# Performance work log

Hardware: AMD Instinct MI355X
Metric: run time of the kernel (lower is better)

Reference implementation:

```python
import jax, jax.numpy as jnp
import numpy as np

T1, T2 = 10.0, 50.0          # Canny hysteresis thresholds from EdgeNorm
HYST_ITERS = 16              # fixed-iteration approximation of Canny hysteresis BFS
TEMPERATURE = 1.0
NUM_CLASSES_M1 = 13.0


def _shift(a, dy, dx):
    # zero-padded shift of [n,h,w]
    p = jnp.pad(a, ((0, 0), (1, 1), (1, 1)))
    return jax.lax.dynamic_slice(p, (0, 1 + dy, 1 + dx), a.shape)


def _sobel(img):
    # img: [n,h,w] float32; replicate border, aperture-3 Sobel (cv2.Canny default)
    p = jnp.pad(img, ((0, 0), (1, 1), (1, 1)), mode='edge')[:, None]  # [n,1,h+2,w+2]
    kx = jnp.array([[-1, 0, 1], [-2, 0, 2], [-1, 0, 1]], jnp.float32)
    ky = jnp.array([[-1, -2, -1], [0, 0, 0], [1, 2, 1]], jnp.float32)
    k = jnp.stack([kx, ky])[:, None]                                  # [2,1,3,3]
    g = jax.lax.conv_general_dilated(p, k, (1, 1), 'VALID')           # [n,2,h,w]
    return g[:, 0], g[:, 1]


def _canny(img_u8):
    # vectorized Canny over the batch (cv2 loops per sample on CPU)
    img = img_u8.astype(jnp.float32)
    gx, gy = _sobel(img)
    mag = jnp.abs(gx) + jnp.abs(gy)                 # L1 magnitude (cv2 L2gradient=False)
    ang = jnp.mod(jnp.degrees(jnp.arctan2(gy, gx)), 180.0)
    s0 = (ang < 22.5) | (ang >= 157.5)
    s45 = (ang >= 22.5) & (ang < 67.5)
    s90 = (ang >= 67.5) & (ang < 112.5)
    # non-max suppression: compare along quantized gradient direction
    n1 = jnp.where(s0, _shift(mag, 0, 1),
         jnp.where(s45, _shift(mag, -1, 1),
         jnp.where(s90, _shift(mag, -1, 0), _shift(mag, -1, -1))))
    n2 = jnp.where(s0, _shift(mag, 0, -1),
         jnp.where(s45, _shift(mag, 1, -1),
         jnp.where(s90, _shift(mag, 1, 0), _shift(mag, 1, 1))))
    nms = jnp.where((mag >= n1) & (mag >= n2), mag, 0.0)
    strong = nms > T2
    weak = nms > T1

    def body(_, s):
        grown = jax.lax.reduce_window(s.astype(jnp.float32), -jnp.inf, jax.lax.max,
                                      (1, 3, 3), (1, 1, 1),
                                      [(0, 0), (1, 1), (1, 1)]) > 0.0
        return grown & weak

    strong = jax.lax.fori_loop(0, HYST_ITERS, body, strong)
    return strong.astype(jnp.float32) * 255.0       # [n,h,w] in {0,255}


def _dilate_blur(edges):
    # cv2.dilate with 10x10 ones kernel, anchor=(5,5) -> asymmetric (5,4) window pad
    d = jax.lax.reduce_window(edges, -jnp.inf, jax.lax.max,
                              (1, 10, 10), (1, 1, 1),
                              [(0, 0), (5, 4), (5, 4)])
    # cv2.blur 10x10 box filter, reflect101 border, rounded back to uint8
    p = jnp.pad(d, ((0, 0), (5, 4), (5, 4)), mode='reflect')
    b = jax.lax.reduce_window(p, 0.0, jax.lax.add,
                              (1, 10, 10), (1, 1, 1), 'VALID') / 100.0
    return jnp.round(b) / 255.0                     # EdgeNorm: e / 255


def setup_inputs() -> dict:
    key = jax.random.key(0)
    k1, k2 = jax.random.split(key)
    n, c, h, w = 8, 14, 512, 512
    return {
        'preds_S': jax.random.normal(k1, (n, c, h, w), dtype=jnp.float32),
        'preds_T': jax.random.normal(k2, (n, c, h, w), dtype=jnp.float32),
    }


def reference(preds_S, preds_T):
    n, c, h, w = preds_S.shape
    # teacher argmax map -> uint8 grayscale (truncating cast, as torch .type(uint8))
    t_map = (jnp.argmax(preds_T, axis=1).astype(jnp.float32)
             / NUM_CLASSES_M1 * 255.0).astype(jnp.uint8)
    edges = jax.lax.stop_gradient(_dilate_blur(_canny(t_map)))  # [n,h,w], constant wrt grads
    pred_T = edges[:, None] * preds_T
    pred_S = edges[:, None] * preds_S
    # ChannelNorm: softmax over flattened h*w per (n,c); divergence='kl' -> norm_s.log()
    logsm_t = jax.nn.log_softmax(pred_T.reshape(n, c, h * w), axis=-1)
    logsm_s = jax.nn.log_softmax(pred_S.reshape(n, c, h * w), axis=-1)
    norm_t = jnp.exp(logsm_t)
    loss = jnp.sum(norm_t * (logsm_t - logsm_s))    # KLDivLoss(reduction='sum')
    loss = loss / (n * c)                           # channel norm divisor
    return loss * (TEMPERATURE ** 2)
```

## Files before the change

kernel.cpp:

```cpp
#include <hip/hip_runtime.h>
#include <math.h>

#define NB 8
#define CC 14
#define HH 512
#define WW 512
#define HW (HH*WW)
#define NHW (NB*HW)
#define WPR 8
#define WPI (HH*WPR)
#define KSPLIT 32
#define KCHUNK (HW/KSPLIT)

typedef unsigned long long u64;

__global__ __launch_bounds__(256) void k_argmax(const float* __restrict__ T,
                                                uchar4* __restrict__ tmap4) {
    int i4 = blockIdx.x * blockDim.x + threadIdx.x;
    if (i4 >= NHW / 4) return;
    int n  = i4 / (HW / 4);
    int p4 = i4 - n * (HW / 4);
    const float4* base = (const float4*)(T + (size_t)n * CC * HW) + p4;
    float4 best = base[0];
    int b0 = 0, b1 = 0, b2 = 0, b3 = 0;
#pragma unroll
    for (int c = 1; c < CC; ++c) {
        float4 v = base[(size_t)c * (HW / 4)];
        if (v.x > best.x) { best.x = v.x; b0 = c; }
        if (v.y > best.y) { best.y = v.y; b1 = c; }
        if (v.z > best.z) { best.z = v.z; b2 = c; }
        if (v.w > best.w) { best.w = v.w; b3 = c; }
    }
    uchar4 g;
    g.x = (unsigned char)(((float)b0 / 13.0f) * 255.0f);
    g.y = (unsigned char)(((float)b1 / 13.0f) * 255.0f);
    g.z = (unsigned char)(((float)b2 / 13.0f) * 255.0f);
    g.w = (unsigned char)(((float)b3 / 13.0f) * 255.0f);
    tmap4[i4] = g;
}

__global__ __launch_bounds__(256) void k_sobel_nms(const unsigned char* __restrict__ tmap,
                                                   u64* __restrict__ weakBits,
                                                   u64* __restrict__ strongBits) {
    int tx = blockIdx.x, ty = blockIdx.y, n = blockIdx.z;
    int x0 = tx * 64, y0 = ty * 64;
    __shared__ unsigned char tm[68 * 68];
    __shared__ unsigned short ms[66 * 66];
    int tid = threadIdx.x;
    const unsigned char* im = tmap + (size_t)n * HW;

    for (int idx = tid; idx < 68 * 68; idx += 256) {
        int r = idx / 68, c = idx - r * 68;
        int yy = y0 - 2 + r; yy = yy < 0 ? 0 : (yy > HH - 1 ? HH - 1 : yy);
        int xx = x0 - 2 + c; xx = xx < 0 ? 0 : (xx > WW - 1 ? WW - 1 : xx);
        tm[idx] = im[yy * WW + xx];
    }
    __syncthreads();

    for (int idx = tid; idx < 66 * 66; idx += 256) {
        int r = idx / 66, c = idx - r * 66;
        const unsigned char* t0 = tm + r * 68 + c;
        int a00 = t0[0],   a01 = t0[1],   a02 = t0[2];
        int a10 = t0[68],                 a12 = t0[70];
        int a20 = t0[136], a21 = t0[137], a22 = t0[138];
        int gx = (a02 - a00) + 2 * (a12 - a10) + (a22 - a20);
        int gy = (a20 - a00) + 2 * (a21 - a01) + (a22 - a02);
        int m = (gx < 0 ? -gx : gx) + (gy < 0 ? -gy : gy);
        float ang = atan2f((float)gy, (float)gx) * 57.29577951308232f;
        ang = fmodf(ang, 180.0f);
        if (ang < 0.0f) ang += 180.0f;
        int s;
        if (ang < 22.5f || ang >= 157.5f) s = 0;
        else if (ang < 67.5f)             s = 1;
        else if (ang < 112.5f)            s = 2;
        else                              s = 3;
        ms[idx] = (unsigned short)((m << 2) | s);
    }
    __syncthreads();

    int lane = tid & 63;
    int warp = tid >> 6;
#pragma unroll
    for (int it = 0; it < 16; ++it) {
        int row = it * 4 + warp;
        int gy_ = y0 + row, gx_ = x0 + lane;
        int v = ms[(row + 1) * 66 + (lane + 1)];
        int mc = v >> 2, s = v & 3;
        int dy1, dx1, dy2, dx2;
        if (s == 0)      { dy1 = 0;  dx1 = 1;  dy2 = 0; dx2 = -1; }
        else if (s == 1) { dy1 = -1; dx1 = 1;  dy2 = 1; dx2 = -1; }
        else if (s == 2) { dy1 = -1; dx1 = 0;  dy2 = 1; dx2 = 0;  }
        else             { dy1 = -1; dx1 = -1; dy2 = 1; dx2 = 1;  }
        int y1 = gy_ + dy1, x1 = gx_ + dx1, y2 = gy_ + dy2, x2 = gx_ + dx2;
        int n1 = (y1 < 0 || y1 >= HH || x1 < 0 || x1 >= WW)
                 ? 0 : (ms[(row + 1 + dy1) * 66 + (lane + 1 + dx1)] >> 2);
        int n2 = (y2 < 0 || y2 >= HH || x2 < 0 || x2 >= WW)
                 ? 0 : (ms[(row + 1 + dy2) * 66 + (lane + 1 + dx2)] >> 2);
        int nms = (mc >= n1 && mc >= n2) ? mc : 0;
        u64 wm = __ballot(nms > 10);
        u64 sm = __ballot(nms > 50);
        if (lane == 0) {
            size_t w = (size_t)n * WPI + gy_ * WPR + tx;
            weakBits[w]   = wm;
            strongBits[w] = sm;
        }
    }
}

#define TR 8
#define HALO 26
#define TROWS (TR + 2*HALO)
#define TWORDS (TROWS * WPR)
#define HYST_THREADS 512
__global__ __launch_bounds__(HYST_THREADS) void k_hyst_dil_blur(const u64* __restrict__ strongBits,
                                                                const u64* __restrict__ weakBits,
                                                                unsigned char* __restrict__ E) {
    int tile = blockIdx.x & 63;
    int n    = blockIdx.x >> 6;
    int t0r  = tile * TR;
    int g0   = t0r - HALO;
    __shared__ u64 A[TWORDS];
    __shared__ u64 B[TWORDS];
    __shared__ u64 Wl[TWORDS];
    __shared__ unsigned char rc[(TR + 10) * 512];
    int tid = threadIdx.x;

    u64 wk = 0;
    if (tid < TWORDS) {
        int vr = g0 + (tid >> 3);
        int w  = tid & 7;
        u64 sv = 0, wv = 0;
        if (vr >= 0 && vr < HH) {
            sv = strongBits[(size_t)n * WPI + vr * WPR + w];
            wv = weakBits  [(size_t)n * WPI + vr * WPR + w];
        }
        A[tid] = sv;
        Wl[tid] = wv;
        wk = wv;
    }
    __syncthreads();

#pragma unroll 1
    for (int it = 0; it < 16; ++it) {
        const u64* src = (it & 1) ? B : A;
        u64*       dst = (it & 1) ? A : B;
        if (tid < TWORDS) {
            int r = tid >> 3;
            int w = tid & 7;
            u64 c  = src[tid];
            u64 up = (r > 0)         ? src[tid - 8] : 0;
            u64 dn = (r < TROWS - 1) ? src[tid + 8] : 0;
            u64 a = c | up | dn;
            u64 pL = 0, pR = 0;
            if (w > 0) {
                u64 cl = src[tid - 1];
                u64 ul = (r > 0)         ? src[tid - 9] : 0;
                u64 dl = (r < TROWS - 1) ? src[tid + 7] : 0;
                pL = cl | ul | dl;
            }
            if (w < 7) {
                u64 cr = src[tid + 1];
                u64 ur = (r > 0)         ? src[tid - 7] : 0;
                u64 dr = (r < TROWS - 1) ? src[tid + 9] : 0;
                pR = cr | ur | dr;
            }
            u64 g = a | (a << 1) | (pL >> 63) | (a >> 1) | (pR << 63);
            dst[tid] = g & wk;
        }
        __syncthreads();
    }

    if (tid < TWORDS) {
        int w = tid & 7;
        u64 v  = A[tid];
        u64 p  = (w > 0) ? A[tid - 1] : 0;
        u64 nx = (w < 7) ? A[tid + 1] : 0;
        u64 o = v;
#pragma unroll
        for (int d = 1; d <= 5; ++d) o |= (v << d) | (p >> (64 - d));
#pragma unroll
        for (int d = 1; d <= 4; ++d) o |= (v >> d) | (nx << (64 - d));
        B[tid] = o;
    }
    __syncthreads();

    u64* D = Wl;
    if (tid < (TR + 10) * WPR) {
        int d = tid >> 3;
        int w = tid & 7;
        int r = d + HALO - 5;
        u64 o = 0;
#pragma unroll
        for (int dy = -5; dy <= 4; ++dy) o |= B[(r + dy) * WPR + w];
        D[d * WPR + w] = o;
    }
    __syncthreads();

    for (int idx = tid; idx < (TR + 10) * 512; idx += HYST_THREADS) {
        int r = idx >> 9;
        int x = idx & 511;
        int c;
        if (x >= 5 && x <= 507) {
            int b = x - 5, wd = b >> 6, off = b & 63;
            u64 v = D[r * WPR + wd] >> off;
            if (off && wd < 7) v |= D[r * WPR + wd + 1] << (64 - off);
            c = __popcll(v & 0x3FFull);
        } else {
            c = 0;
            for (int dx = -5; dx <= 4; ++dx) {
                int xx = x + dx;
                xx = xx < 0 ? -xx : (xx > WW - 1 ? 2 * (WW - 1) - xx : xx);
                c += (int)((D[r * WPR + (xx >> 6)] >> (xx & 63)) & 1ull);
            }
        }
        rc[idx] = (unsigned char)c;
    }
    __syncthreads();

    for (int idx = tid; idx < TR * 512; idx += HYST_THREADS) {
        int yy = idx >> 9;
        int x  = idx & 511;
        int gy = t0r + yy;
        int sum = 0;
        if (gy >= 5 && gy <= HH - 5) {
#pragma unroll
            for (int k = 0; k < 10; ++k) sum += rc[(yy + k) * 512 + x];
        } else {
#pragma unroll
            for (int k = 0; k < 10; ++k) {
                int v  = gy - 5 + k;
                int rv = v < 0 ? -v : (v > HH - 1 ? 2 * (HH - 1) - v : v);
                sum += rc[(rv - (t0r - 5)) * 512 + x];
            }
        }
        float b = rintf((255.0f * (float)sum) / 100.0f);
        E[(size_t)n * HW + gy * WW + x] = (unsigned char)b;
    }
}

__global__ __launch_bounds__(256) void k_kl_partial(const float* __restrict__ S,
                                                    const float* __restrict__ T,
                                                    const unsigned char* __restrict__ E,
                                                    double* __restrict__ partial) {
    int cidx  = blockIdx.x;
    int split = blockIdx.y;
    int n = cidx / CC;
    const float4* Tp = (const float4*)(T + (size_t)cidx * HW + (size_t)split * KCHUNK);
    const float4* Sp = (const float4*)(S + (size_t)cidx * HW + (size_t)split * KCHUNK);
    const uchar4* Ep = (const uchar4*)(E + (size_t)n    * HW + (size_t)split * KCHUNK);
    int tid = threadIdx.x;

    float Zt = 0.0f, Wt = 0.0f, Zs = 0.0f;
#pragma unroll
    for (int k = 0; k < KCHUNK / 4 / 256; ++k) {
        int j = k * 256 + tid;
        float4 t4 = Tp[j];
        float4 s4 = Sp[j];
        uchar4 e4 = Ep[j];
#pragma unroll
        for (int u = 0; u < 4; ++u) {
            float e = (float)((&e4.x)[u]) / 255.0f;
            float t = e * (&t4.x)[u];
            float s = e * (&s4.x)[u];
            float et = __expf(t);
            Zt += et;
            Wt += et * (t - s);
            Zs += __expf(s);
        }
    }

    double zt = (double)Zt, wt = (double)Wt, zs = (double)Zs;
#pragma unroll
    for (int off = 32; off > 0; off >>= 1) {
        zt += __shfl_down(zt, off);
        wt += __shfl_down(wt, off);
        zs += __shfl_down(zs, off);
    }
    __shared__ double wr[4][3];
    int wv = tid >> 6, ln = tid & 63;
    if (ln == 0) { wr[wv][0] = zt; wr[wv][1] = wt; wr[wv][2] = zs; }
    __syncthreads();
    if (tid == 0) {
        double* o = partial + ((size_t)cidx * KSPLIT + split) * 3;
        o[0] = wr[0][0] + wr[1][0] + wr[2][0] + wr[3][0];
        o[1] = wr[0][1] + wr[1][1] + wr[2][1] + wr[3][1];
        o[2] = wr[0][2] + wr[1][2] + wr[2][2] + wr[3][2];
    }
}

__global__ __launch_bounds__(128) void k_kl_final(const double* __restrict__ partial,
                                                  float* __restrict__ out) {
    int tid = threadIdx.x;
    double loss = 0.0;
    if (tid < NB * CC) {
        double Zt = 0.0, Wt = 0.0, Zs = 0.0;
        for (int sp = 0; sp < KSPLIT; ++sp) {
            const double* p = partial + ((size_t)tid * KSPLIT + sp) * 3;
            Zt += p[0]; Wt += p[1]; Zs += p[2];
        }
        loss = Wt / Zt - log(Zt) + log(Zs);
    }
    __shared__ double red[128];
    red[tid] = loss;
    __syncthreads();
    for (int off = 64; off > 0; off >>= 1) {
        if (tid < off) red[tid] += red[tid + off];
        __syncthreads();
    }
    if (tid == 0) out[0] = (float)(red[0] / (double)(NB * CC));
}

extern "C" void kernel_launch(void* const* d_in, const int* in_sizes, int n_in,
                              void* d_out, int out_size, void* d_ws, size_t ws_size,
                              hipStream_t stream) {
    const float* S = (const float*)d_in[0];
    const float* T = (const float*)d_in[1];
    float* out = (float*)d_out;

    char* ws = (char*)d_ws;
    unsigned char* e_buf      = (unsigned char*)(ws);
    unsigned char* tmap       = (unsigned char*)(ws + (size_t)NHW);
    u64*           weakBits   = (u64*)(ws + (size_t)NHW * 2);
    u64*           strongBits = (u64*)(ws + (size_t)NHW * 2 + (NHW/8));
    double*        partial    = (double*)(ws + (size_t)NHW * 2 + 2*(NHW/8));

    k_argmax<<<dim3(NHW / 4 / 256), dim3(256), 0, stream>>>(T, (uchar4*)tmap);
    k_sobel_nms<<<dim3(8, 8, NB), dim3(256), 0, stream>>>(tmap, weakBits, strongBits);
    k_hyst_dil_blur<<<dim3(NB * 64), dim3(HYST_THREADS), 0, stream>>>(strongBits, weakBits, e_buf);
    k_kl_partial<<<dim3(NB * CC, KSPLIT), dim3(256), 0, stream>>>(S, T, e_buf, partial);
    k_kl_final<<<1, 128, 0, stream>>>(partial, out);
    (void)in_sizes; (void)n_in; (void)out_size; (void)ws_size;
}
```

Before: 303.9 us.

## Fuse argmax into Sobel/NMS, enlarge hysteresis tiles, use LUT for edge scale

After: 292.9 us. 1.04x faster.

```diff
diff --git a/kernel.cpp b/kernel.cpp
--- a/kernel.cpp
+++ b/kernel.cpp
@@ -14,46 +14,29 @@
 
 typedef unsigned long long u64;
 
-__global__ __launch_bounds__(256) void k_argmax(const float* __restrict__ T,
-                                                uchar4* __restrict__ tmap4) {
-    int i4 = blockIdx.x * blockDim.x + threadIdx.x;
-    if (i4 >= NHW / 4) return;
-    int n  = i4 / (HW / 4);
-    int p4 = i4 - n * (HW / 4);
-    const float4* base = (const float4*)(T + (size_t)n * CC * HW) + p4;
-    float4 best = base[0];
-    int b0 = 0, b1 = 0, b2 = 0, b3 = 0;
-#pragma unroll
-    for (int c = 1; c < CC; ++c) {
-        float4 v = base[(size_t)c * (HW / 4)];
-        if (v.x > best.x) { best.x = v.x; b0 = c; }
-        if (v.y > best.y) { best.y = v.y; b1 = c; }
-        if (v.z > best.z) { best.z = v.z; b2 = c; }
-        if (v.w > best.w) { best.w = v.w; b3 = c; }
-    }
-    uchar4 g;
-    g.x = (unsigned char)(((float)b0 / 13.0f) * 255.0f);
-    g.y = (unsigned char)(((float)b1 / 13.0f) * 255.0f);
-    g.z = (unsigned char)(((float)b2 / 13.0f) * 255.0f);
-    g.w = (unsigned char)(((float)b3 / 13.0f) * 255.0f);
-    tmap4[i4] = g;
-}
-
-__global__ __launch_bounds__(256) void k_sobel_nms(const unsigned char* __restrict__ tmap,
-                                                   u64* __restrict__ weakBits,
-                                                   u64* __restrict__ strongBits) {
+__global__ __launch_bounds__(256) void k_front(const float* __restrict__ T,
+                                               u64* __restrict__ weakBits,
+                                               u64* __restrict__ strongBits) {
     int tx = blockIdx.x, ty = blockIdx.y, n = blockIdx.z;
     int x0 = tx * 64, y0 = ty * 64;
     __shared__ unsigned char tm[68 * 68];
     __shared__ unsigned short ms[66 * 66];
     int tid = threadIdx.x;
-    const unsigned char* im = tmap + (size_t)n * HW;
+    const float* Tb = T + (size_t)n * CC * HW;
 
     for (int idx = tid; idx < 68 * 68; idx += 256) {
         int r = idx / 68, c = idx - r * 68;
         int yy = y0 - 2 + r; yy = yy < 0 ? 0 : (yy > HH - 1 ? HH - 1 : yy);
         int xx = x0 - 2 + c; xx = xx < 0 ? 0 : (xx > WW - 1 ? WW - 1 : xx);
-        tm[idx] = im[yy * WW + xx];
+        const float* p = Tb + yy * WW + xx;
+        float best = p[0];
+        int bi = 0;
+#pragma unroll
+        for (int ch = 1; ch < CC; ++ch) {
+            float v = p[(size_t)ch * HW];
+            if (v > best) { best = v; bi = ch; }
+        }
+        tm[idx] = (unsigned char)((bi * 255) / 13);
     }
     __syncthreads();
 
@@ -107,71 +90,63 @@
     }
 }
 
-#define TR 8
-#define HALO 26
+#define TR 16
+#define HALO 28
 #define TROWS (TR + 2*HALO)
 #define TWORDS (TROWS * WPR)
-#define HYST_THREADS 512
+#define DROWS (TR + 10)
+#define HYST_THREADS 576
 __global__ __launch_bounds__(HYST_THREADS) void k_hyst_dil_blur(const u64* __restrict__ strongBits,
                                                                 const u64* __restrict__ weakBits,
                                                                 unsigned char* __restrict__ E) {
-    int tile = blockIdx.x & 63;
-    int n    = blockIdx.x >> 6;
+    int tile = blockIdx.x & 31;
+    int n    = blockIdx.x >> 5;
     int t0r  = tile * TR;
     int g0   = t0r - HALO;
     __shared__ u64 A[TWORDS];
     __shared__ u64 B[TWORDS];
-    __shared__ u64 Wl[TWORDS];
-    __shared__ unsigned char rc[(TR + 10) * 512];
+    __shared__ unsigned char rc[DROWS * 512];
     int tid = threadIdx.x;
-
-    u64 wk = 0;
-    if (tid < TWORDS) {
-        int vr = g0 + (tid >> 3);
-        int w  = tid & 7;
-        u64 sv = 0, wv = 0;
-        if (vr >= 0 && vr < HH) {
-            sv = strongBits[(size_t)n * WPI + vr * WPR + w];
-            wv = weakBits  [(size_t)n * WPI + vr * WPR + w];
-        }
-        A[tid] = sv;
-        Wl[tid] = wv;
-        wk = wv;
-    }
+    int r = tid >> 3;
+    int w = tid & 7;
+
+    int vr = g0 + r;
+    u64 sv = 0, wk = 0;
+    if (vr >= 0 && vr < HH) {
+        sv = strongBits[(size_t)n * WPI + vr * WPR + w];
+        wk = weakBits  [(size_t)n * WPI + vr * WPR + w];
+    }
+    A[tid] = sv;
     __syncthreads();
 
 #pragma unroll 1
     for (int it = 0; it < 16; ++it) {
         const u64* src = (it & 1) ? B : A;
         u64*       dst = (it & 1) ? A : B;
-        if (tid < TWORDS) {
-            int r = tid >> 3;
-            int w = tid & 7;
-            u64 c  = src[tid];
-            u64 up = (r > 0)         ? src[tid - 8] : 0;
-            u64 dn = (r < TROWS - 1) ? src[tid + 8] : 0;
-            u64 a = c | up | dn;
-            u64 pL = 0, pR = 0;
-            if (w > 0) {
-                u64 cl = src[tid - 1];
-                u64 ul = (r > 0)         ? src[tid - 9] : 0;
-                u64 dl = (r < TROWS - 1) ? src[tid + 7] : 0;
-                pL = cl | ul | dl;
-            }
-            if (w < 7) {
-                u64 cr = src[tid + 1];
-                u64 ur = (r > 0)         ? src[tid - 7] : 0;
-                u64 dr = (r < TROWS - 1) ? src[tid + 9] : 0;
-                pR = cr | ur | dr;
-            }
-            u64 g = a | (a << 1) | (pL >> 63) | (a >> 1) | (pR << 63);
-            dst[tid] = g & wk;
-        }
+        u64 c  = src[tid];
+        u64 up = (r > 0)         ? src[tid - 8] : 0;
+        u64 dn = (r < TROWS - 1) ? src[tid + 8] : 0;
+        u64 a = c | up | dn;
+        u64 pL = 0, pR = 0;
+        if (w > 0) {
+            u64 cl = src[tid - 1];
+            u64 ul = (r > 0)         ? src[tid - 9] : 0;
+            u64 dl = (r < TROWS - 1) ? src[tid + 7] : 0;
+            pL = cl | ul | dl;
+        }
+        if (w < 7) {
+            u64 cr = src[tid + 1];
+            u64 ur = (r > 0)         ? src[tid - 7] : 0;
+            u64 dr = (r < TROWS - 1) ? src[tid + 9] : 0;
+            pR = cr | ur | dr;
+        }
+        u64 g = a | (a << 1) | (pL >> 63) | (a >> 1) | (pR << 63);
         __syncthreads();
-    }
-
-    if (tid < TWORDS) {
-        int w = tid & 7;
+        dst[tid] = g & wk;
+        __syncthreads();
+    }
+
+    {
         u64 v  = A[tid];
         u64 p  = (w > 0) ? A[tid - 1] : 0;
         u64 nx = (w < 7) ? A[tid + 1] : 0;
@@ -180,37 +155,37 @@
         for (int d = 1; d <= 5; ++d) o |= (v << d) | (p >> (64 - d));
 #pragma unroll
         for (int d = 1; d <= 4; ++d) o |= (v >> d) | (nx << (64 - d));
+        __syncthreads();
         B[tid] = o;
     }
     __syncthreads();
 
-    u64* D = Wl;
-    if (tid < (TR + 10) * WPR) {
-        int d = tid >> 3;
-        int w = tid & 7;
-        int r = d + HALO - 5;
+    u64* D = A;
+    if (tid < DROWS * WPR) {
+        int d  = tid >> 3;
+        int rr = d + HALO - 5;
         u64 o = 0;
 #pragma unroll
-        for (int dy = -5; dy <= 4; ++dy) o |= B[(r + dy) * WPR + w];
+        for (int dy = -5; dy <= 4; ++dy) o |= B[(rr + dy) * WPR + w];
         D[d * WPR + w] = o;
     }
     __syncthreads();
 
-    for (int idx = tid; idx < (TR + 10) * 512; idx += HYST_THREADS) {
-        int r = idx >> 9;
-        int x = idx & 511;
+    for (int idx = tid; idx < DROWS * 512; idx += HYST_THREADS) {
+        int rr = idx >> 9;
+        int x  = idx & 511;
         int c;
         if (x >= 5 && x <= 507) {
             int b = x - 5, wd = b >> 6, off = b & 63;
-            u64 v = D[r * WPR + wd] >> off;
-            if (off && wd < 7) v |= D[r * WPR + wd + 1] << (64 - off);
+            u64 v = D[rr * WPR + wd] >> off;
+            if (off && wd < 7) v |= D[rr * WPR + wd + 1] << (64 - off);
             c = __popcll(v & 0x3FFull);
         } else {
             c = 0;
             for (int dx = -5; dx <= 4; ++dx) {
                 int xx = x + dx;
                 xx = xx < 0 ? -xx : (xx > WW - 1 ? 2 * (WW - 1) - xx : xx);
-                c += (int)((D[r * WPR + (xx >> 6)] >> (xx & 63)) & 1ull);
+                c += (int)((D[rr * WPR + (xx >> 6)] >> (xx & 63)) & 1ull);
             }
         }
         rc[idx] = (unsigned char)c;
@@ -250,6 +225,10 @@
     const uchar4* Ep = (const uchar4*)(E + (size_t)n    * HW + (size_t)split * KCHUNK);
     int tid = threadIdx.x;
 
+    __shared__ float lut[256];
+    lut[tid] = (float)tid / 255.0f;
+    __syncthreads();
+
     float Zt = 0.0f, Wt = 0.0f, Zs = 0.0f;
 #pragma unroll
     for (int k = 0; k < KCHUNK / 4 / 256; ++k) {
@@ -259,7 +238,7 @@
         uchar4 e4 = Ep[j];
 #pragma unroll
         for (int u = 0; u < 4; ++u) {
-            float e = (float)((&e4.x)[u]) / 255.0f;
+            float e = lut[(&e4.x)[u]];
             float t = e * (&t4.x)[u];
             float s = e * (&s4.x)[u];
             float et = __expf(t);
@@ -319,14 +298,12 @@
 
     char* ws = (char*)d_ws;
     unsigned char* e_buf      = (unsigned char*)(ws);
-    unsigned char* tmap       = (unsigned char*)(ws + (size_t)NHW);
-    u64*           weakBits   = (u64*)(ws + (size_t)NHW * 2);
-    u64*           strongBits = (u64*)(ws + (size_t)NHW * 2 + (NHW/8));
-    double*        partial    = (double*)(ws + (size_t)NHW * 2 + 2*(NHW/8));
-
-    k_argmax<<<dim3(NHW / 4 / 256), dim3(256), 0, stream>>>(T, (uchar4*)tmap);
-    k_sobel_nms<<<dim3(8, 8, NB), dim3(256), 0, stream>>>(tmap, weakBits, strongBits);
-    k_hyst_dil_blur<<<dim3(NB * 64), dim3(HYST_THREADS), 0, stream>>>(strongBits, weakBits, e_buf);
+    u64*           weakBits   = (u64*)(ws + (size_t)NHW);
+    u64*           strongBits = (u64*)(ws + (size_t)NHW + (NHW/8));
+    double*        partial    = (double*)(ws + (size_t)NHW + 2*(NHW/8));
+
+    k_front<<<dim3(8, 8, NB), dim3(256), 0, stream>>>(T, weakBits, strongBits);
+    k_hyst_dil_blur<<<dim3(NB * 32), dim3(HYST_THREADS), 0, stream>>>(strongBits, weakBits, e_buf);
     k_kl_partial<<<dim3(NB * CC, KSPLIT), dim3(256), 0, stream>>>(S, T, e_buf, partial);
     k_kl_final<<<1, 128, 0, stream>>>(partial, out);
     (void)in_sizes; (void)n_in; (void)out_size; (void)ws_size;
```
